# Performance work log

Hardware: AMD Instinct MI355X
Metric: run time of the kernel (lower is better)

Reference implementation:

```python
import jax, jax.numpy as jnp
import numpy as np

B_, T_, IDIM, D, H, FF, L, MAXLEN = 8, 512, 1799, 256, 4, 2048, 16, 1000
DK = D // H


def _ln(x, g, b, eps=1e-12):
    m = jnp.mean(x, axis=-1, keepdims=True)
    v = jnp.mean((x - m) ** 2, axis=-1, keepdims=True)
    return (x - m) * jax.lax.rsqrt(v + eps) * g + b


def setup_inputs() -> dict:
    key = jax.random.key(0)
    ks = jax.random.split(key, 16)
    s = 0.02
    n = lambda k, shape: jax.random.normal(k, shape, jnp.float32) * s
    return {
        'xs': jax.random.normal(ks[0], (B_, T_, IDIM), jnp.float32),
        'masks': jnp.ones((B_, 1, T_), jnp.int32),
        'emb_w': n(ks[1], (D, IDIM)), 'emb_b': jnp.zeros((D,), jnp.float32),
        'emb_g': jnp.ones((D,), jnp.float32), 'emb_beta': jnp.zeros((D,), jnp.float32),
        'pe_k': n(ks[2], (2 * MAXLEN, DK)),
        'Wq': n(ks[3], (L, D, D)), 'bq': jnp.zeros((L, D), jnp.float32),
        'Wk': n(ks[4], (L, D, D)), 'bk': jnp.zeros((L, D), jnp.float32),
        'Wv': n(ks[5], (L, D, D)), 'bv': jnp.zeros((L, D), jnp.float32),
        'Wo': n(ks[6], (L, D, D)), 'bo': jnp.zeros((L, D), jnp.float32),
        'ln1_g': jnp.ones((L, D), jnp.float32), 'ln1_b': jnp.zeros((L, D), jnp.float32),
        'ln2_g': jnp.ones((L, D), jnp.float32), 'ln2_b': jnp.zeros((L, D), jnp.float32),
        'lnk_g': jnp.ones((L, DK), jnp.float32), 'lnk_b': jnp.zeros((L, DK), jnp.float32),
        'W1': n(ks[7], (L, FF, D)), 'b1': jnp.zeros((L, FF), jnp.float32),
        'W2': n(ks[8], (L, D, FF)), 'b2': jnp.zeros((L, D), jnp.float32),
        'after_g': jnp.ones((D,), jnp.float32), 'after_b': jnp.zeros((D,), jnp.float32),
    }


def reference(xs, masks, emb_w, emb_b, emb_g, emb_beta, pe_k, Wq, bq, Wk, bk, Wv, bv, Wo, bo,
              ln1_g, ln1_b, ln2_g, ln2_b, lnk_g, lnk_b, W1, b1, W2, b2, after_g, after_b):
    # embed: Linear -> LayerNorm -> (Dropout=id) -> ReLU
    x = jax.nn.relu(_ln(xs @ emb_w.T + emb_b, emb_g, emb_beta))  # [B,T,D]
    # relative position table gather: pos_k [T,T,DK]
    pos = jnp.arange(T_)
    rel = jnp.clip(pos[:, None] - pos[None, :], -MAXLEN, MAXLEN - 1) + MAXLEN
    pos_k = pe_k[rel]
    neg = (masks == 0)[:, None, :, :]  # [B,1,1,T]
    minval = jnp.finfo(x.dtype).min
    scale = 1.0 / np.sqrt(DK).astype(np.float32)

    def block(x, p):
        y = _ln(x, p['ln1_g'], p['ln1_b'])
        pk = _ln(pos_k, p['lnk_g'], p['lnk_b'])  # norm_k applied per layer
        proj = lambda W, b: (y @ W.T + b).reshape(B_, T_, H, DK).transpose(0, 2, 1, 3)
        q = proj(p['Wq'], p['bq'])  # [B,H,T,DK]
        k = proj(p['Wk'], p['bk'])
        v = proj(p['Wv'], p['bv'])
        A = jnp.einsum('bhtd,bhsd->bhts', q, k)
        Bt = jnp.einsum('bhtd,tsd->bhts', q, pk)  # rel-pos bias term
        scores = jnp.where(neg, minval, (A + Bt) * scale)
        attn = jnp.where(neg, 0.0, jax.nn.softmax(scores, axis=-1))
        o = jnp.einsum('bhts,bhsd->bhtd', attn, v)
        o = o.transpose(0, 2, 1, 3).reshape(B_, T_, D)
        x = x + o @ p['Wo'].T + p['bo']
        y2 = _ln(x, p['ln2_g'], p['ln2_b'])
        ff = jax.nn.relu(y2 @ p['W1'].T + p['b1']) @ p['W2'].T + p['b2']
        return x + ff, None

    params = {'Wq': Wq, 'bq': bq, 'Wk': Wk, 'bk': bk, 'Wv': Wv, 'bv': bv, 'Wo': Wo, 'bo': bo,
              'ln1_g': ln1_g, 'ln1_b': ln1_b, 'ln2_g': ln2_g, 'ln2_b': ln2_b,
              'lnk_g': lnk_g, 'lnk_b': lnk_b, 'W1': W1, 'b1': b1, 'W2': W2, 'b2': b2}
    x, _ = jax.lax.scan(block, x, params)
    return _ln(x, after_g, after_b)
```

## Files before the change

kernel.cpp:

```cpp
#include <hip/hip_runtime.h>
#include <cstdint>


typedef __bf16 bf16_t;
typedef bf16_t bf16x4 __attribute__((ext_vector_type(4)));
typedef bf16_t bf16x8 __attribute__((ext_vector_type(8)));
typedef float  f32x4  __attribute__((ext_vector_type(4)));

#define B_    8
#define T_    512
#define IDIM  1799
#define KPAD  1856
#define D_    256
#define H_    4
#define DK    64
#define FF_   2048
#define L_    16
#define NROW  4096
#define PKROWS 2000
#define NBH   32
#define NSA   4

__device__ __forceinline__ f32x4 mfma16(bf16x8 a, bf16x8 b, f32x4 c) {
  return __builtin_amdgcn_mfma_f32_16x16x32_bf16(a, b, c, 0, 0, 0);
}

__device__ __forceinline__ void async_cp16(const void* g, void* l) {
  __builtin_amdgcn_global_load_lds(
      (__attribute__((address_space(1))) void*)(g),
      (__attribute__((address_space(3))) void*)(l), 16, 0, 0);
}

__global__ __launch_bounds__(256) void cvt_f32_bf16(const float* __restrict__ s,
                                                    bf16_t* __restrict__ d, int n) {
  int i = blockIdx.x * 256 + threadIdx.x;
  int stride = gridDim.x * 256;
  for (; i < n; i += stride) d[i] = (bf16_t)s[i];
}

__global__ __launch_bounds__(256) void cvt_pad_row(const float* __restrict__ s,
                                                   bf16_t* __restrict__ d,
                                                   int ksrc, int kdst) {
  const int r = blockIdx.x;
  const float* sr = s + (size_t)r * ksrc;
  bf16_t* dr = d + (size_t)r * kdst;
  for (int k = threadIdx.x; k < kdst; k += 256)
    dr[k] = (k < ksrc) ? (bf16_t)sr[k] : (bf16_t)0.f;
}

__global__ __launch_bounds__(256) void pack_qkvw(const float* __restrict__ wq,
                                                 const float* __restrict__ wk,
                                                 const float* __restrict__ wv,
                                                 bf16_t* __restrict__ dst) {
  const int per_l = 768 * 256;
  int i = blockIdx.x * 256 + threadIdx.x;
  int stride = gridDim.x * 256;
  for (; i < L_ * per_l; i += stride) {
    int l = i / per_l, r = i - l * per_l;
    int n = r >> 8, c = r & 255;
    int sel = n >> 8, nn = n & 255;
    const float* w = (sel == 0) ? wq : (sel == 1) ? wk : wv;
    dst[i] = (bf16_t)w[((size_t)l * 256 + nn) * 256 + c];
  }
}

__global__ __launch_bounds__(256) void pack_qkvb(const float* __restrict__ bq,
                                                 const float* __restrict__ bk,
                                                 const float* __restrict__ bv,
                                                 float* __restrict__ dst) {
  int i = blockIdx.x * 256 + threadIdx.x;
  if (i >= L_ * 768) return;
  int l = i / 768, n = i - l * 768;
  int sel = n >> 8, nn = n & 255;
  const float* b = (sel == 0) ? bq : (sel == 1) ? bk : bv;
  dst[i] = b[l * 256 + nn];
}

__global__ __launch_bounds__(256) void pkn_ln(const float* __restrict__ pe_k,
                                              const float* __restrict__ lnk_g,
                                              const float* __restrict__ lnk_b,
                                              bf16_t* __restrict__ out) {
  const int idx = blockIdx.x * 4 + (threadIdx.x >> 6);
  if (idx >= L_ * PKROWS) return;
  const int lane = threadIdx.x & 63;
  const int l = idx / PKROWS, r = idx - l * PKROWS;
  float v = pe_k[(size_t)r * DK + lane];
  float s = v;
#pragma unroll
  for (int o = 32; o; o >>= 1) s += __shfl_xor(s, o);
  const float mean = s * (1.f / DK);
  const float dx = v - mean;
  float q = dx * dx;
#pragma unroll
  for (int o = 32; o; o >>= 1) q += __shfl_xor(q, o);
  const float rs = rsqrtf(q * (1.f / DK) + 1e-12f);
  out[((size_t)l * PKROWS + r) * DK + lane] =
      (bf16_t)(dx * rs * lnk_g[l * DK + lane] + lnk_b[l * DK + lane]);
}

template <bool BF16OUT, bool RELU>
__global__ __launch_bounds__(256) void ln_rows(const float* __restrict__ src,
                                               const float* __restrict__ g,
                                               const float* __restrict__ b,
                                               void* __restrict__ dst) {
  const int row = blockIdx.x * 4 + (threadIdx.x >> 6);
  const int lane = threadIdx.x & 63;
  const float4 v = ((const float4*)(src + (size_t)row * D_))[lane];
  float s = v.x + v.y + v.z + v.w;
#pragma unroll
  for (int o = 32; o; o >>= 1) s += __shfl_xor(s, o);
  const float mean = s * (1.f / D_);
  const float d0 = v.x - mean, d1 = v.y - mean, d2 = v.z - mean, d3 = v.w - mean;
  float q = d0 * d0 + d1 * d1 + d2 * d2 + d3 * d3;
#pragma unroll
  for (int o = 32; o; o >>= 1) q += __shfl_xor(q, o);
  const float rs = rsqrtf(q * (1.f / D_) + 1e-12f);
  const float4 gg = ((const float4*)g)[lane];
  const float4 bb = ((const float4*)b)[lane];
  float o0 = d0 * rs * gg.x + bb.x;
  float o1 = d1 * rs * gg.y + bb.y;
  float o2 = d2 * rs * gg.z + bb.z;
  float o3 = d3 * rs * gg.w + bb.w;
  if (RELU) {
    o0 = fmaxf(o0, 0.f); o1 = fmaxf(o1, 0.f);
    o2 = fmaxf(o2, 0.f); o3 = fmaxf(o3, 0.f);
  }
  if (BF16OUT) {
    bf16x4 o4 = {(bf16_t)o0, (bf16_t)o1, (bf16_t)o2, (bf16_t)o3};
    ((bf16x4*)((bf16_t*)dst + (size_t)row * D_))[lane] = o4;
  } else {
    ((float4*)((float*)dst + (size_t)row * D_))[lane] = make_float4(o0, o1, o2, o3);
  }
}

template <int NS, bool WRITE_Y>
__global__ __launch_bounds__(256) void add_combine_ln(
    const float* __restrict__ parts, const float* __restrict__ bias,
    float* __restrict__ x, const float* __restrict__ g,
    const float* __restrict__ b, bf16_t* __restrict__ y) {
  const int row = blockIdx.x * 4 + (threadIdx.x >> 6);
  const int lane = threadIdx.x & 63;
  const size_t idx = (size_t)row * 64 + lane;
  float4 v = ((const float4*)x)[idx];
#pragma unroll
  for (int p = 0; p < NS; ++p) {
    float4 pv = ((const float4*)parts)[(size_t)p * NROW * 64 + idx];
    v.x += pv.x; v.y += pv.y; v.z += pv.z; v.w += pv.w;
  }
  const float4 bi = ((const float4*)bias)[lane];
  v.x += bi.x; v.y += bi.y; v.z += bi.z; v.w += bi.w;
  ((float4*)x)[idx] = v;
  if (WRITE_Y) {
    float s = v.x + v.y + v.z + v.w;
#pragma unroll
    for (int o = 32; o; o >>= 1) s += __shfl_xor(s, o);
    const float mean = s * (1.f / D_);
    const float d0 = v.x - mean, d1 = v.y - mean, d2 = v.z - mean, d3 = v.w - mean;
    float q = d0 * d0 + d1 * d1 + d2 * d2 + d3 * d3;
#pragma unroll
    for (int o = 32; o; o >>= 1) q += __shfl_xor(q, o);
    const float rs = rsqrtf(q * (1.f / D_) + 1e-12f);
    const float4 gg = ((const float4*)g)[lane];
    const float4 bb = ((const float4*)b)[lane];
    bf16x4 o4 = {(bf16_t)(d0 * rs * gg.x + bb.x), (bf16_t)(d1 * rs * gg.y + bb.y),
                 (bf16_t)(d2 * rs * gg.z + bb.z), (bf16_t)(d3 * rs * gg.w + bb.w)};
    ((bf16x4*)y)[idx] = o4;
  }
}

__global__ __launch_bounds__(256) void embed_combine(
    const float* __restrict__ parts, const float* __restrict__ bias,
    const float* __restrict__ g, const float* __restrict__ b,
    float* __restrict__ x) {
  const int row = blockIdx.x * 4 + (threadIdx.x >> 6);
  const int lane = threadIdx.x & 63;
  const size_t idx = (size_t)row * 64 + lane;
  float4 v = ((const float4*)parts)[idx];
  float4 p1 = ((const float4*)parts)[(size_t)NROW * 64 + idx];
  const float4 bi = ((const float4*)bias)[lane];
  v.x += p1.x + bi.x; v.y += p1.y + bi.y; v.z += p1.z + bi.z; v.w += p1.w + bi.w;
  float s = v.x + v.y + v.z + v.w;
#pragma unroll
  for (int o = 32; o; o >>= 1) s += __shfl_xor(s, o);
  const float mean = s * (1.f / D_);
  const float d0 = v.x - mean, d1 = v.y - mean, d2 = v.z - mean, d3 = v.w - mean;
  float q = d0 * d0 + d1 * d1 + d2 * d2 + d3 * d3;
#pragma unroll
  for (int o = 32; o; o >>= 1) q += __shfl_xor(q, o);
  const float rs = rsqrtf(q * (1.f / D_) + 1e-12f);
  const float4 gg = ((const float4*)g)[lane];
  const float4 bb = ((const float4*)b)[lane];
  ((float4*)x)[idx] = make_float4(
      fmaxf(d0 * rs * gg.x + bb.x, 0.f), fmaxf(d1 * rs * gg.y + bb.y, 0.f),
      fmaxf(d2 * rs * gg.z + bb.z, 0.f), fmaxf(d3 * rs * gg.w + bb.w, 0.f));
}

template <int BM, int BN, int EP, int MINW>
__global__ __launch_bounds__(256, MINW) void gemm_bf16(
    const bf16_t* __restrict__ A, int lda, const bf16_t* __restrict__ B, int ldb,
    const float* __restrict__ bias, void* __restrict__ Cout, int ldc,
    const float* __restrict__ resid, int K, size_t zstride) {
  constexpr int HM = BM / 2, HN = BN / 2;
  constexpr int FM = HM / 16, FN = HN / 16;
  constexpr int CA = (BM * 8) / 256, CB = (BN * 8) / 256;
  __shared__ bf16_t lsA[BM * 64];
  __shared__ bf16_t lsB[BN * 64];
  const int tid = threadIdx.x;
  const int w = tid >> 6, lane = tid & 63;
  const int wm = w >> 1, wn = w & 1;
  const int lanelo = lane & 15, quad = lane >> 4;
  const int wbase = tid & ~63;
  const int m0 = blockIdx.x * BM, n0 = blockIdx.y * BN;
  const int ktiles = K >> 6;
  const int tpz = (ktiles + gridDim.z - 1) / gridDim.z;
  const int kb = blockIdx.z * tpz * 64;
  const int ke = min(K, kb + tpz * 64);
  f32x4 acc[FM][FN] = {};

  for (int kt = kb; kt < ke; kt += 64) {
    __syncthreads();
#pragma unroll
    for (int rr = 0; rr < CA; ++rr) {
      int chunk = rr * 256 + tid;
      int r = chunk >> 3, c8 = chunk & 7;
      int lg = c8 ^ (r & 7);
      async_cp16(A + (size_t)(m0 + r) * lda + kt + lg * 8,
                 lsA + (size_t)(rr * 256 + wbase) * 8);
    }
#pragma unroll
    for (int rr = 0; rr < CB; ++rr) {
      int chunk = rr * 256 + tid;
      int r = chunk >> 3, c8 = chunk & 7;
      int lg = c8 ^ (r & 7);
      async_cp16(B + (size_t)(n0 + r) * ldb + kt + lg * 8,
                 lsB + (size_t)(rr * 256 + wbase) * 8);
    }
    __syncthreads();
    bf16x8 af[FM][2], bfv[FN][2];
#pragma unroll
    for (int i = 0; i < FM; ++i) {
      int r = wm * HM + i * 16 + lanelo;
#pragma unroll
      for (int kk = 0; kk < 2; ++kk)
        af[i][kk] = *(const bf16x8*)(lsA + (size_t)(r * 8 + ((kk * 4 + quad) ^ (r & 7))) * 8);
    }
#pragma unroll
    for (int j = 0; j < FN; ++j) {
      int r = wn * HN + j * 16 + lanelo;
#pragma unroll
      for (int kk = 0; kk < 2; ++kk)
        bfv[j][kk] = *(const bf16x8*)(lsB + (size_t)(r * 8 + ((kk * 4 + quad) ^ (r & 7))) * 8);
    }
#pragma unroll
    for (int kk = 0; kk < 2; ++kk)
#pragma unroll
      for (int i = 0; i < FM; ++i)
#pragma unroll
        for (int j = 0; j < FN; ++j)
          acc[i][j] = mfma16(af[i][kk], bfv[j][kk], acc[i][j]);
  }

#pragma unroll
  for (int i = 0; i < FM; ++i) {
#pragma unroll
    for (int j = 0; j < FN; ++j) {
#pragma unroll
      for (int reg = 0; reg < 4; ++reg) {
        const int m = m0 + wm * HM + i * 16 + quad * 4 + reg;
        const int n = n0 + wn * HN + j * 16 + lanelo;
        const size_t idx = (size_t)m * ldc + n;
        if constexpr (EP == 4) {
          ((float*)Cout + (size_t)blockIdx.z * zstride)[idx] = acc[i][j][reg];
        } else {
          float v = acc[i][j][reg] + bias[n];
          if constexpr (EP == 0) {
            ((float*)Cout)[idx] = v;
          } else if constexpr (EP == 1) {
            ((bf16_t*)Cout)[idx] = (bf16_t)v;
          } else if constexpr (EP == 2) {
            ((bf16_t*)Cout)[idx] = (bf16_t)fmaxf(v, 0.f);
          } else {
            ((float*)Cout)[idx] = v + resid[idx];
          }
        }
      }
    }
  }
}

__global__ __launch_bounds__(256, 3) void bt_gemm(
    const bf16_t* __restrict__ qkv, const bf16_t* __restrict__ pkn,
    bf16_t* __restrict__ Bt) {
  __shared__ bf16_t ls_q[64 * 64];
  __shared__ bf16_t ls_j[192 * 64];
  const int tid = threadIdx.x, w = tid >> 6, lane = tid & 63;
  const int wm = w >> 1, wn = w & 1;
  const int lanelo = lane & 15, quad = lane >> 4;
  const int wbase = tid & ~63;
  const int t0 = blockIdx.x * 64;
  const int bh = blockIdx.y, bb = bh >> 2, h = bh & 3;
  const size_t rowbase = (size_t)bb * T_;
  const int relbase = t0 + 489;

#pragma unroll
  for (int rr = 0; rr < 2; ++rr) {
    int chunk = rr * 256 + tid;
    int r = chunk >> 3, c8 = chunk & 7;
    int lg = c8 ^ (r & 7);
    async_cp16(qkv + (rowbase + t0 + r) * 768 + h * 64 + lg * 8,
               ls_q + (size_t)(rr * 256 + wbase) * 8);
  }
  __syncthreads();
  bf16x8 qf[2][2];
#pragma unroll
  for (int i = 0; i < 2; ++i) {
    int r = wm * 32 + i * 16 + lanelo;
#pragma unroll
    for (int kk = 0; kk < 2; ++kk)
      qf[i][kk] = *(const bf16x8*)(ls_q + (size_t)(r * 8 + ((kk * 4 + quad) ^ (r & 7))) * 8);
  }

  for (int jc = 0; jc < 3; ++jc) {
    if (jc) __syncthreads();
#pragma unroll
    for (int rr = 0; rr < 6; ++rr) {
      int chunk = rr * 256 + tid;
      int r = chunk >> 3, c8 = chunk & 7;
      int lg = c8 ^ (r & 7);
      async_cp16(pkn + (size_t)(relbase + jc * 192 + r) * DK + lg * 8,
                 ls_j + (size_t)(rr * 256 + wbase) * 8);
    }
    __syncthreads();
    f32x4 racc[2][6] = {};
#pragma unroll
    for (int kk = 0; kk < 2; ++kk)
#pragma unroll
      for (int nf = 0; nf < 6; ++nf) {
        int r = wn * 96 + nf * 16 + lanelo;
        bf16x8 bj = *(const bf16x8*)(ls_j + (size_t)(r * 8 + ((kk * 4 + quad) ^ (r & 7))) * 8);
#pragma unroll
        for (int i = 0; i < 2; ++i) racc[i][nf] = mfma16(qf[i][kk], bj, racc[i][nf]);
      }
#pragma unroll
    for (int i = 0; i < 2; ++i)
#pragma unroll
      for (int nf = 0; nf < 6; ++nf)
#pragma unroll
        for (int reg = 0; reg < 4; ++reg) {
          const int tl = wm * 32 + i * 16 + quad * 4 + reg;
          const int jj = jc * 192 + wn * 96 + nf * 16 + lanelo;
          const int s = tl + 511 - jj;
          if (s >= 0 && s < T_)
            Bt[(((size_t)bh * T_ + t0 + tl) << 9) + s] = (bf16_t)racc[i][nf][reg];
        }
  }
}

__global__ __launch_bounds__(256, 4) void attn_part(
    const bf16_t* __restrict__ qkv, const bf16_t* __restrict__ Bt,
    const int* __restrict__ masks, bf16_t* __restrict__ Opart,
    float* __restrict__ mpart, float* __restrict__ lpart) {
  __shared__ bf16_t ls_q[64 * 64];
  __shared__ bf16_t ls_k[64 * 64];
  __shared__ bf16_t ls_vt[64 * 72];
  __shared__ bf16_t ls_p[64 * 72];

  const int tid = threadIdx.x, w = tid >> 6, lane = tid & 63;
  const int lanelo = lane & 15, quad = lane >> 4;
  const int wbase = tid & ~63;
  const int t0 = blockIdx.x * 64;
  const int bh = blockIdx.y, bb = bh >> 2, h = bh & 3;
  const int z = blockIdx.z;
  const size_t rowbase = (size_t)bb * T_;

#pragma unroll
  for (int rr = 0; rr < 2; ++rr) {
    int chunk = rr * 256 + tid;
    int r = chunk >> 3, c8 = chunk & 7;
    int lg = c8 ^ (r & 7);
    async_cp16(qkv + (rowbase + t0 + r) * 768 + h * 64 + lg * 8,
               ls_q + (size_t)(rr * 256 + wbase) * 8);
  }
  __syncthreads();
  bf16x8 qf[2];
#pragma unroll
  for (int kk = 0; kk < 2; ++kk) {
    int r = w * 16 + lanelo;
    qf[kk] = *(const bf16x8*)(ls_q + (size_t)(r * 8 + ((kk * 4 + quad) ^ (r & 7))) * 8);
  }

  f32x4 o_acc[4] = {};
  float m_run[4], l_run[4];
#pragma unroll
  for (int i = 0; i < 4; ++i) { m_run[i] = -__builtin_inff(); l_run[i] = 0.f; }

  for (int st = 2 * z; st < 2 * z + 2; ++st) {
    const int s0 = st * 64;
    __syncthreads();
#pragma unroll
    for (int rr = 0; rr < 2; ++rr) {
      int chunk = rr * 256 + tid;
      int r = chunk >> 3, c8 = chunk & 7;
      int lg = c8 ^ (r & 7);
      async_cp16(qkv + (rowbase + s0 + r) * 768 + 256 + h * 64 + lg * 8,
                 ls_k + (size_t)(rr * 256 + wbase) * 8);
    }
#pragma unroll
    for (int c = tid; c < 64 * 8; c += 256) {
      int r = c & 63, d0 = (c >> 6) * 8;
      bf16x8 vv = *(const bf16x8*)(qkv + (rowbase + s0 + r) * 768 + 512 + h * 64 + d0);
#pragma unroll
      for (int i = 0; i < 8; ++i) ls_vt[(d0 + i) * 72 + r] = vv[i];
    }
    __syncthreads();

    float btv[4][4];
    int mk[4];
#pragma unroll
    for (int nf = 0; nf < 4; ++nf) {
      const int scol = nf * 16 + lanelo;
      mk[nf] = masks[bb * T_ + s0 + scol];
#pragma unroll
      for (int reg = 0; reg < 4; ++reg) {
        const int trow = w * 16 + quad * 4 + reg;
        btv[nf][reg] = (float)Bt[(((size_t)bh * T_ + t0 + trow) << 9) + s0 + scol];
      }
    }
    f32x4 sacc[4] = {};
#pragma unroll
    for (int kk = 0; kk < 2; ++kk)
#pragma unroll
      for (int nf = 0; nf < 4; ++nf) {
        int r = nf * 16 + lanelo;
        bf16x8 bk = *(const bf16x8*)(ls_k + (size_t)(r * 8 + ((kk * 4 + quad) ^ (r & 7))) * 8);
        sacc[nf] = mfma16(qf[kk], bk, sacc[nf]);
      }
    float sv[4][4];
#pragma unroll
    for (int nf = 0; nf < 4; ++nf)
#pragma unroll
      for (int reg = 0; reg < 4; ++reg)
        sv[nf][reg] = mk[nf] ? (sacc[nf][reg] + btv[nf][reg]) * 0.125f
                             : -3.4028235e38f;
    float alpha[4];
#pragma unroll
    for (int reg = 0; reg < 4; ++reg) {
      float bm = fmaxf(fmaxf(sv[0][reg], sv[1][reg]), fmaxf(sv[2][reg], sv[3][reg]));
#pragma unroll
      for (int o = 1; o < 16; o <<= 1) bm = fmaxf(bm, __shfl_xor(bm, o));
      const float mn = fmaxf(m_run[reg], bm);
      alpha[reg] = __expf(m_run[reg] - mn);
      m_run[reg] = mn;
      float rsum = 0.f;
#pragma unroll
      for (int nf = 0; nf < 4; ++nf) {
        float p = __expf(sv[nf][reg] - mn) * (mk[nf] ? 1.f : 0.f);
        sv[nf][reg] = p;
        rsum += p;
      }
#pragma unroll
      for (int o = 1; o < 16; o <<= 1) rsum += __shfl_xor(rsum, o);
      l_run[reg] = l_run[reg] * alpha[reg] + rsum;
    }
#pragma unroll
    for (int nf = 0; nf < 4; ++nf)
#pragma unroll
      for (int reg = 0; reg < 4; ++reg) {
        o_acc[nf][reg] *= alpha[reg];
        ls_p[(w * 16 + quad * 4 + reg) * 72 + nf * 16 + lanelo] = (bf16_t)sv[nf][reg];
      }
#pragma unroll
    for (int kk = 0; kk < 2; ++kk) {
      bf16x8 ap = *(const bf16x8*)&ls_p[(w * 16 + lanelo) * 72 + kk * 32 + quad * 8];
#pragma unroll
      for (int nf = 0; nf < 4; ++nf) {
        bf16x8 bv = *(const bf16x8*)&ls_vt[(nf * 16 + lanelo) * 72 + kk * 32 + quad * 8];
        o_acc[nf] = mfma16(ap, bv, o_acc[nf]);
      }
    }
  }

#pragma unroll
  for (int reg = 0; reg < 4; ++reg) {
    const int trow = w * 16 + quad * 4 + reg;
    const size_t prow = ((size_t)z * NBH + bh) * T_ + t0 + trow;
#pragma unroll
    for (int nf = 0; nf < 4; ++nf)
      Opart[prow * 64 + nf * 16 + lanelo] = (bf16_t)o_acc[nf][reg];
    if (lanelo == 0) { mpart[prow] = m_run[reg]; lpart[prow] = l_run[reg]; }
  }
}

__global__ __launch_bounds__(256) void attn_combine(
    const bf16_t* __restrict__ Opart, const float* __restrict__ mpart,
    const float* __restrict__ lpart, bf16_t* __restrict__ ao) {
  const int hr = blockIdx.x * 4 + (threadIdx.x >> 6);
  const int lane = threadIdx.x & 63;
  const int bh = hr >> 9, t = hr & 511;
  float mp[NSA], lp[NSA];
  float m = -__builtin_inff();
#pragma unroll
  for (int p = 0; p < NSA; ++p) {
    const size_t prow = ((size_t)p * NBH + bh) * T_ + t;
    mp[p] = mpart[prow]; lp[p] = lpart[prow];
    m = fmaxf(m, mp[p]);
  }
  float denom = 0.f, o = 0.f;
#pragma unroll
  for (int p = 0; p < NSA; ++p) {
    if (lp[p] > 0.f) {
      const float wp = __expf(mp[p] - m);
      denom += lp[p] * wp;
      o += (float)Opart[(((size_t)p * NBH + bh) * T_ + t) * 64 + lane] * wp;
    }
  }
  const float res = (denom > 0.f) ? o / denom : 0.f;
  const int bb = bh >> 2, hh = bh & 3;
  ao[((size_t)bb * T_ + t) * D_ + hh * 64 + lane] = (bf16_t)res;
}

extern "C" void kernel_launch(void* const* d_in, const int* in_sizes, int n_in,
                              void* d_out, int out_size, void* d_ws, size_t ws_size,
                              hipStream_t stream) {
  const float* xs       = (const float*)d_in[0];
  const int*   masks    = (const int*)d_in[1];
  const float* emb_w    = (const float*)d_in[2];
  const float* emb_b    = (const float*)d_in[3];
  const float* emb_g    = (const float*)d_in[4];
  const float* emb_beta = (const float*)d_in[5];
  const float* pe_k     = (const float*)d_in[6];
  const float* Wq       = (const float*)d_in[7];
  const float* bq       = (const float*)d_in[8];
  const float* Wk       = (const float*)d_in[9];
  const float* bk       = (const float*)d_in[10];
  const float* Wv       = (const float*)d_in[11];
  const float* bv       = (const float*)d_in[12];
  const float* Wo       = (const float*)d_in[13];
  const float* bo       = (const float*)d_in[14];
  const float* ln1_g    = (const float*)d_in[15];
  const float* ln1_b    = (const float*)d_in[16];
  const float* ln2_g    = (const float*)d_in[17];
  const float* ln2_b    = (const float*)d_in[18];
  const float* lnk_g    = (const float*)d_in[19];
  const float* lnk_b    = (const float*)d_in[20];
  const float* W1       = (const float*)d_in[21];
  const float* b1       = (const float*)d_in[22];
  const float* W2       = (const float*)d_in[23];
  const float* b2       = (const float*)d_in[24];
  const float* after_g  = (const float*)d_in[25];
  const float* after_b  = (const float*)d_in[26];

  char* ws = (char*)d_ws;
  size_t off = 0;
  auto take = [&](size_t bytes) -> void* {
    void* p = ws + off;
    off += (bytes + 255) & ~(size_t)255;
    return p;
  };
  bf16_t* ewb  = (bf16_t*)take((size_t)D_ * KPAD * 2);
  bf16_t* wcat = (bf16_t*)take((size_t)L_ * 768 * D_ * 2);
  float*  bcat = (float*) take((size_t)L_ * 768 * 4);
  bf16_t* wob  = (bf16_t*)take((size_t)L_ * D_ * D_ * 2);
  bf16_t* w1b  = (bf16_t*)take((size_t)L_ * FF_ * D_ * 2);
  bf16_t* w2b  = (bf16_t*)take((size_t)L_ * D_ * FF_ * 2);
  bf16_t* pknb = (bf16_t*)take((size_t)L_ * PKROWS * DK * 2);
  float*  x    = (float*) take((size_t)NROW * D_ * 4);
  bf16_t* y    = (bf16_t*)take((size_t)NROW * D_ * 2);
  bf16_t* qkv  = (bf16_t*)take((size_t)NROW * 768 * 2);
  bf16_t* ao   = (bf16_t*)take((size_t)NROW * D_ * 2);
  bf16_t* hbuf = (bf16_t*)take((size_t)NROW * FF_ * 2);
  bf16_t* Btb  = (bf16_t*)take((size_t)NBH * T_ * T_ * 2);
  bf16_t* Opart = (bf16_t*)take((size_t)NSA * NBH * T_ * 64 * 2);
  float*  mpart = (float*)take((size_t)NSA * NBH * T_ * 4);
  float*  lpart = (float*)take((size_t)NSA * NBH * T_ * 4);
  float*  gpart = (float*)take((size_t)2 * NROW * D_ * 4);
  bf16_t* xsb  = hbuf;
  const size_t ZS = (size_t)NROW * D_;

  cvt_pad_row<<<NROW, 256, 0, stream>>>(xs, xsb, IDIM, KPAD);
  cvt_pad_row<<<D_, 256, 0, stream>>>(emb_w, ewb, IDIM, KPAD);
  pack_qkvw<<<2048, 256, 0, stream>>>(Wq, Wk, Wv, wcat);
  pack_qkvb<<<48, 256, 0, stream>>>(bq, bk, bv, bcat);
  cvt_f32_bf16<<<1024, 256, 0, stream>>>(Wo, wob, L_ * D_ * D_);
  cvt_f32_bf16<<<2048, 256, 0, stream>>>(W1, w1b, L_ * FF_ * D_);
  cvt_f32_bf16<<<2048, 256, 0, stream>>>(W2, w2b, L_ * D_ * FF_);
  pkn_ln<<<(L_ * PKROWS) / 4, 256, 0, stream>>>(pe_k, lnk_g, lnk_b, pknb);

  gemm_bf16<64, 64, 4, 3><<<dim3(NROW / 64, D_ / 64, 2), 256, 0, stream>>>(
      xsb, KPAD, ewb, KPAD, nullptr, gpart, D_, nullptr, KPAD, ZS);
  embed_combine<<<NROW / 4, 256, 0, stream>>>(gpart, emb_b, emb_g, emb_beta, x);
  ln_rows<true, false><<<NROW / 4, 256, 0, stream>>>(x, ln1_g, ln1_b, y);

  for (int l = 0; l < L_; ++l) {
    gemm_bf16<64, 64, 1, 3><<<dim3(NROW / 64, 768 / 64), 256, 0, stream>>>(
        y, D_, wcat + (size_t)l * 768 * D_, D_, bcat + l * 768, qkv, 768, nullptr,
        D_, 0);
    bt_gemm<<<dim3(T_ / 64, NBH), 256, 0, stream>>>(
        qkv, pknb + (size_t)l * PKROWS * DK, Btb);
    attn_part<<<dim3(T_ / 64, NBH, NSA), 256, 0, stream>>>(
        qkv, Btb, masks, Opart, mpart, lpart);
    attn_combine<<<NBH * T_ / 4, 256, 0, stream>>>(Opart, mpart, lpart, ao);
    gemm_bf16<64, 64, 4, 3><<<dim3(NROW / 64, D_ / 64, 2), 256, 0, stream>>>(
        ao, D_, wob + (size_t)l * D_ * D_, D_, nullptr, gpart, D_, nullptr, D_, ZS);
    add_combine_ln<2, true><<<NROW / 4, 256, 0, stream>>>(
        gpart, bo + l * D_, x, ln2_g + l * D_, ln2_b + l * D_, y);
    gemm_bf16<128, 128, 2, 2><<<dim3(NROW / 128, FF_ / 128), 256, 0, stream>>>(
        y, D_, w1b + (size_t)l * FF_ * D_, D_, b1 + l * FF_, hbuf, FF_, nullptr,
        D_, 0);
    gemm_bf16<64, 64, 4, 3><<<dim3(NROW / 64, D_ / 64, 2), 256, 0, stream>>>(
        hbuf, FF_, w2b + (size_t)l * D_ * FF_, FF_, nullptr, gpart, D_, nullptr,
        FF_, ZS);
    if (l < L_ - 1) {
      add_combine_ln<2, true><<<NROW / 4, 256, 0, stream>>>(
          gpart, b2 + l * D_, x, ln1_g + (l + 1) * D_, ln1_b + (l + 1) * D_, y);
    } else {
      add_combine_ln<2, false><<<NROW / 4, 256, 0, stream>>>(
          gpart, b2 + l * D_, x, nullptr, nullptr, nullptr);
    }
  }
  ln_rows<false, false><<<NROW / 4, 256, 0, stream>>>(x, after_g, after_b,
                                                      (float*)d_out);
}
```

Baseline: 1.436 ms.

## Fuse rel-pos bias into attention, fold combine into Wo GEMM, retile GEMMs

```diff
diff --git a/kernel.cpp b/kernel.cpp
--- a/kernel.cpp
+++ b/kernel.cpp
@@ -98,11 +98,10 @@
       (bf16_t)(dx * rs * lnk_g[l * DK + lane] + lnk_b[l * DK + lane]);
 }
 
-template <bool BF16OUT, bool RELU>
-__global__ __launch_bounds__(256) void ln_rows(const float* __restrict__ src,
-                                               const float* __restrict__ g,
-                                               const float* __restrict__ b,
-                                               void* __restrict__ dst) {
+__global__ __launch_bounds__(256) void ln_rows_f32(const float* __restrict__ src,
+                                                   const float* __restrict__ g,
+                                                   const float* __restrict__ b,
+                                                   float* __restrict__ dst) {
   const int row = blockIdx.x * 4 + (threadIdx.x >> 6);
   const int lane = threadIdx.x & 63;
   const float4 v = ((const float4*)(src + (size_t)row * D_))[lane];
@@ -117,20 +116,9 @@
   const float rs = rsqrtf(q * (1.f / D_) + 1e-12f);
   const float4 gg = ((const float4*)g)[lane];
   const float4 bb = ((const float4*)b)[lane];
-  float o0 = d0 * rs * gg.x + bb.x;
-  float o1 = d1 * rs * gg.y + bb.y;
-  float o2 = d2 * rs * gg.z + bb.z;
-  float o3 = d3 * rs * gg.w + bb.w;
-  if (RELU) {
-    o0 = fmaxf(o0, 0.f); o1 = fmaxf(o1, 0.f);
-    o2 = fmaxf(o2, 0.f); o3 = fmaxf(o3, 0.f);
-  }
-  if (BF16OUT) {
-    bf16x4 o4 = {(bf16_t)o0, (bf16_t)o1, (bf16_t)o2, (bf16_t)o3};
-    ((bf16x4*)((bf16_t*)dst + (size_t)row * D_))[lane] = o4;
-  } else {
-    ((float4*)((float*)dst + (size_t)row * D_))[lane] = make_float4(o0, o1, o2, o3);
-  }
+  ((float4*)(dst + (size_t)row * D_))[lane] =
+      make_float4(d0 * rs * gg.x + bb.x, d1 * rs * gg.y + bb.y,
+                  d2 * rs * gg.z + bb.z, d3 * rs * gg.w + bb.w);
 }
 
 template <int NS, bool WRITE_Y>
@@ -170,36 +158,57 @@
 
 __global__ __launch_bounds__(256) void embed_combine(
     const float* __restrict__ parts, const float* __restrict__ bias,
-    const float* __restrict__ g, const float* __restrict__ b,
-    float* __restrict__ x) {
+    const float* __restrict__ g0, const float* __restrict__ b0,
+    const float* __restrict__ g1, const float* __restrict__ b1,
+    float* __restrict__ x, bf16_t* __restrict__ y) {
   const int row = blockIdx.x * 4 + (threadIdx.x >> 6);
   const int lane = threadIdx.x & 63;
   const size_t idx = (size_t)row * 64 + lane;
   float4 v = ((const float4*)parts)[idx];
-  float4 p1 = ((const float4*)parts)[(size_t)NROW * 64 + idx];
+#pragma unroll
+  for (int p = 1; p < 4; ++p) {
+    float4 pv = ((const float4*)parts)[(size_t)p * NROW * 64 + idx];
+    v.x += pv.x; v.y += pv.y; v.z += pv.z; v.w += pv.w;
+  }
   const float4 bi = ((const float4*)bias)[lane];
-  v.x += p1.x + bi.x; v.y += p1.y + bi.y; v.z += p1.z + bi.z; v.w += p1.w + bi.w;
+  v.x += bi.x; v.y += bi.y; v.z += bi.z; v.w += bi.w;
   float s = v.x + v.y + v.z + v.w;
 #pragma unroll
   for (int o = 32; o; o >>= 1) s += __shfl_xor(s, o);
-  const float mean = s * (1.f / D_);
-  const float d0 = v.x - mean, d1 = v.y - mean, d2 = v.z - mean, d3 = v.w - mean;
+  float mean = s * (1.f / D_);
+  float d0 = v.x - mean, d1 = v.y - mean, d2 = v.z - mean, d3 = v.w - mean;
   float q = d0 * d0 + d1 * d1 + d2 * d2 + d3 * d3;
 #pragma unroll
   for (int o = 32; o; o >>= 1) q += __shfl_xor(q, o);
-  const float rs = rsqrtf(q * (1.f / D_) + 1e-12f);
-  const float4 gg = ((const float4*)g)[lane];
-  const float4 bb = ((const float4*)b)[lane];
-  ((float4*)x)[idx] = make_float4(
-      fmaxf(d0 * rs * gg.x + bb.x, 0.f), fmaxf(d1 * rs * gg.y + bb.y, 0.f),
-      fmaxf(d2 * rs * gg.z + bb.z, 0.f), fmaxf(d3 * rs * gg.w + bb.w, 0.f));
+  float rs = rsqrtf(q * (1.f / D_) + 1e-12f);
+  const float4 gg = ((const float4*)g0)[lane];
+  const float4 bb = ((const float4*)b0)[lane];
+  float x0 = fmaxf(d0 * rs * gg.x + bb.x, 0.f);
+  float x1 = fmaxf(d1 * rs * gg.y + bb.y, 0.f);
+  float x2 = fmaxf(d2 * rs * gg.z + bb.z, 0.f);
+  float x3 = fmaxf(d3 * rs * gg.w + bb.w, 0.f);
+  ((float4*)x)[idx] = make_float4(x0, x1, x2, x3);
+  s = x0 + x1 + x2 + x3;
+#pragma unroll
+  for (int o = 32; o; o >>= 1) s += __shfl_xor(s, o);
+  mean = s * (1.f / D_);
+  d0 = x0 - mean; d1 = x1 - mean; d2 = x2 - mean; d3 = x3 - mean;
+  q = d0 * d0 + d1 * d1 + d2 * d2 + d3 * d3;
+#pragma unroll
+  for (int o = 32; o; o >>= 1) q += __shfl_xor(q, o);
+  rs = rsqrtf(q * (1.f / D_) + 1e-12f);
+  const float4 g1v = ((const float4*)g1)[lane];
+  const float4 b1v = ((const float4*)b1)[lane];
+  bf16x4 o4 = {(bf16_t)(d0 * rs * g1v.x + b1v.x), (bf16_t)(d1 * rs * g1v.y + b1v.y),
+               (bf16_t)(d2 * rs * g1v.z + b1v.z), (bf16_t)(d3 * rs * g1v.w + b1v.w)};
+  ((bf16x4*)y)[idx] = o4;
 }
 
 template <int BM, int BN, int EP, int MINW>
 __global__ __launch_bounds__(256, MINW) void gemm_bf16(
     const bf16_t* __restrict__ A, int lda, const bf16_t* __restrict__ B, int ldb,
     const float* __restrict__ bias, void* __restrict__ Cout, int ldc,
-    const float* __restrict__ resid, int K, size_t zstride) {
+    int K, size_t zstride) {
   constexpr int HM = BM / 2, HN = BN / 2;
   constexpr int FM = HM / 16, FN = HN / 16;
   constexpr int CA = (BM * 8) / 256, CB = (BN * 8) / 256;
@@ -273,14 +282,10 @@
           ((float*)Cout + (size_t)blockIdx.z * zstride)[idx] = acc[i][j][reg];
         } else {
           float v = acc[i][j][reg] + bias[n];
-          if constexpr (EP == 0) {
-            ((float*)Cout)[idx] = v;
-          } else if constexpr (EP == 1) {
+          if constexpr (EP == 1) {
             ((bf16_t*)Cout)[idx] = (bf16_t)v;
-          } else if constexpr (EP == 2) {
+          } else {
             ((bf16_t*)Cout)[idx] = (bf16_t)fmaxf(v, 0.f);
-          } else {
-            ((float*)Cout)[idx] = v + resid[idx];
           }
         }
       }
@@ -288,82 +293,114 @@
   }
 }
 
-__global__ __launch_bounds__(256, 3) void bt_gemm(
-    const bf16_t* __restrict__ qkv, const bf16_t* __restrict__ pkn,
-    bf16_t* __restrict__ Bt) {
-  __shared__ bf16_t ls_q[64 * 64];
-  __shared__ bf16_t ls_j[192 * 64];
-  const int tid = threadIdx.x, w = tid >> 6, lane = tid & 63;
+__global__ __launch_bounds__(256, 2) void wo_gemm(
+    const bf16_t* __restrict__ Opart, const float* __restrict__ mpart,
+    const float* __restrict__ lpart, const bf16_t* __restrict__ B,
+    float* __restrict__ Cout, size_t zstride) {
+  __shared__ bf16_t lsA[64 * 64];
+  __shared__ bf16_t lsB[128 * 64];
+  const int tid = threadIdx.x;
+  const int w = tid >> 6, lane = tid & 63;
   const int wm = w >> 1, wn = w & 1;
   const int lanelo = lane & 15, quad = lane >> 4;
   const int wbase = tid & ~63;
-  const int t0 = blockIdx.x * 64;
-  const int bh = blockIdx.y, bb = bh >> 2, h = bh & 3;
-  const size_t rowbase = (size_t)bb * T_;
-  const int relbase = t0 + 489;
-
-#pragma unroll
-  for (int rr = 0; rr < 2; ++rr) {
-    int chunk = rr * 256 + tid;
-    int r = chunk >> 3, c8 = chunk & 7;
-    int lg = c8 ^ (r & 7);
-    async_cp16(qkv + (rowbase + t0 + r) * 768 + h * 64 + lg * 8,
-               ls_q + (size_t)(rr * 256 + wbase) * 8);
-  }
-  __syncthreads();
-  bf16x8 qf[2][2];
-#pragma unroll
-  for (int i = 0; i < 2; ++i) {
-    int r = wm * 32 + i * 16 + lanelo;
-#pragma unroll
-    for (int kk = 0; kk < 2; ++kk)
-      qf[i][kk] = *(const bf16x8*)(ls_q + (size_t)(r * 8 + ((kk * 4 + quad) ^ (r & 7))) * 8);
-  }
-
-  for (int jc = 0; jc < 3; ++jc) {
-    if (jc) __syncthreads();
-#pragma unroll
-    for (int rr = 0; rr < 6; ++rr) {
+  const int m0 = blockIdx.x * 64, n0 = blockIdx.y * 128;
+  const int z = blockIdx.z;
+  const int bb = m0 >> 9, t0 = m0 & 511;
+  f32x4 acc[2][4] = {};
+
+  for (int kt = z * 128; kt < z * 128 + 128; kt += 64) {
+    __syncthreads();
+    const int hh = kt >> 6;
+    const int bh = bb * 4 + hh;
+#pragma unroll
+    for (int rr = 0; rr < 2; ++rr) {
+      int chunk = rr * 256 + tid;
+      int r = chunk >> 3, c8 = chunk & 7;
+      int dk0 = (c8 ^ (r & 7)) * 8;
+      int t = t0 + r;
+      float mp[NSA], lp[NSA];
+      float mmax = -__builtin_inff();
+#pragma unroll
+      for (int p = 0; p < NSA; ++p) {
+        const size_t prow = ((size_t)p * NBH + bh) * T_ + t;
+        mp[p] = mpart[prow]; lp[p] = lpart[prow];
+        mmax = fmaxf(mmax, mp[p]);
+      }
+      float e[NSA], denom = 0.f;
+#pragma unroll
+      for (int p = 0; p < NSA; ++p) {
+        e[p] = __expf(mp[p] - mmax);
+        denom += lp[p] * e[p];
+      }
+      const float inv = (denom > 0.f) ? 1.f / denom : 0.f;
+      float cv[8] = {};
+#pragma unroll
+      for (int p = 0; p < NSA; ++p) {
+        const float wgt = e[p] * inv;
+        bf16x8 op = *(const bf16x8*)(Opart +
+            (((size_t)p * NBH + bh) * T_ + t) * 64 + dk0);
+#pragma unroll
+        for (int i = 0; i < 8; ++i) cv[i] += wgt * (float)op[i];
+      }
+      bf16x8 rv;
+#pragma unroll
+      for (int i = 0; i < 8; ++i) rv[i] = (bf16_t)cv[i];
+      *(bf16x8*)(lsA + (size_t)chunk * 8) = rv;
+    }
+#pragma unroll
+    for (int rr = 0; rr < 4; ++rr) {
       int chunk = rr * 256 + tid;
       int r = chunk >> 3, c8 = chunk & 7;
       int lg = c8 ^ (r & 7);
-      async_cp16(pkn + (size_t)(relbase + jc * 192 + r) * DK + lg * 8,
-                 ls_j + (size_t)(rr * 256 + wbase) * 8);
+      async_cp16(B + (size_t)(n0 + r) * 256 + kt + lg * 8,
+                 lsB + (size_t)(rr * 256 + wbase) * 8);
     }
     __syncthreads();
-    f32x4 racc[2][6] = {};
+    bf16x8 af[2][2], bfv[4][2];
+#pragma unroll
+    for (int i = 0; i < 2; ++i) {
+      int r = wm * 32 + i * 16 + lanelo;
+#pragma unroll
+      for (int kk = 0; kk < 2; ++kk)
+        af[i][kk] = *(const bf16x8*)(lsA + (size_t)(r * 8 + ((kk * 4 + quad) ^ (r & 7))) * 8);
+    }
+#pragma unroll
+    for (int j = 0; j < 4; ++j) {
+      int r = wn * 64 + j * 16 + lanelo;
+#pragma unroll
+      for (int kk = 0; kk < 2; ++kk)
+        bfv[j][kk] = *(const bf16x8*)(lsB + (size_t)(r * 8 + ((kk * 4 + quad) ^ (r & 7))) * 8);
+    }
 #pragma unroll
     for (int kk = 0; kk < 2; ++kk)
 #pragma unroll
-      for (int nf = 0; nf < 6; ++nf) {
-        int r = wn * 96 + nf * 16 + lanelo;
-        bf16x8 bj = *(const bf16x8*)(ls_j + (size_t)(r * 8 + ((kk * 4 + quad) ^ (r & 7))) * 8);
-#pragma unroll
-        for (int i = 0; i < 2; ++i) racc[i][nf] = mfma16(qf[i][kk], bj, racc[i][nf]);
-      }
-#pragma unroll
-    for (int i = 0; i < 2; ++i)
-#pragma unroll
-      for (int nf = 0; nf < 6; ++nf)
-#pragma unroll
-        for (int reg = 0; reg < 4; ++reg) {
-          const int tl = wm * 32 + i * 16 + quad * 4 + reg;
-          const int jj = jc * 192 + wn * 96 + nf * 16 + lanelo;
-          const int s = tl + 511 - jj;
-          if (s >= 0 && s < T_)
-            Bt[(((size_t)bh * T_ + t0 + tl) << 9) + s] = (bf16_t)racc[i][nf][reg];
-        }
-  }
-}
-
-__global__ __launch_bounds__(256, 4) void attn_part(
-    const bf16_t* __restrict__ qkv, const bf16_t* __restrict__ Bt,
+      for (int i = 0; i < 2; ++i)
+#pragma unroll
+        for (int j = 0; j < 4; ++j)
+          acc[i][j] = mfma16(af[i][kk], bfv[j][kk], acc[i][j]);
+  }
+
+#pragma unroll
+  for (int i = 0; i < 2; ++i)
+#pragma unroll
+    for (int j = 0; j < 4; ++j)
+#pragma unroll
+      for (int reg = 0; reg < 4; ++reg) {
+        const int m = m0 + wm * 32 + i * 16 + quad * 4 + reg;
+        const int n = n0 + wn * 64 + j * 16 + lanelo;
+        (Cout + (size_t)z * zstride)[(size_t)m * D_ + n] = acc[i][j][reg];
+      }
+}
+
+__global__ __launch_bounds__(256, 3) void attn_fused(
+    const bf16_t* __restrict__ qkv, const bf16_t* __restrict__ pkn,
     const int* __restrict__ masks, bf16_t* __restrict__ Opart,
     float* __restrict__ mpart, float* __restrict__ lpart) {
-  __shared__ bf16_t ls_q[64 * 64];
+  __shared__ bf16_t ls_qp[64 * 72];
+  __shared__ bf16_t ls_pkr[64 * 196];
   __shared__ bf16_t ls_k[64 * 64];
   __shared__ bf16_t ls_vt[64 * 72];
-  __shared__ bf16_t ls_p[64 * 72];
 
   const int tid = threadIdx.x, w = tid >> 6, lane = tid & 63;
   const int lanelo = lane & 15, quad = lane >> 4;
@@ -372,6 +409,7 @@
   const int bh = blockIdx.y, bb = bh >> 2, h = bh & 3;
   const int z = blockIdx.z;
   const size_t rowbase = (size_t)bb * T_;
+  const int jb = t0 - 128 * z + 873;
 
 #pragma unroll
   for (int rr = 0; rr < 2; ++rr) {
@@ -379,23 +417,47 @@
     int r = chunk >> 3, c8 = chunk & 7;
     int lg = c8 ^ (r & 7);
     async_cp16(qkv + (rowbase + t0 + r) * 768 + h * 64 + lg * 8,
-               ls_q + (size_t)(rr * 256 + wbase) * 8);
+               ls_qp + (size_t)(rr * 256 + wbase) * 8);
+  }
+#pragma unroll
+  for (int rr = 0; rr < 6; ++rr) {
+    int chunk = rr * 256 + tid;
+    int r = chunk >> 3, c8 = chunk & 7;
+    int lg = c8 ^ (r & 7);
+    async_cp16(pkn + (size_t)(jb + r) * DK + lg * 8,
+               ls_pkr + (size_t)(rr * 256 + wbase) * 8);
   }
   __syncthreads();
   bf16x8 qf[2];
 #pragma unroll
   for (int kk = 0; kk < 2; ++kk) {
     int r = w * 16 + lanelo;
-    qf[kk] = *(const bf16x8*)(ls_q + (size_t)(r * 8 + ((kk * 4 + quad) ^ (r & 7))) * 8);
-  }
+    qf[kk] = *(const bf16x8*)(ls_qp + (size_t)(r * 8 + ((kk * 4 + quad) ^ (r & 7))) * 8);
+  }
+  f32x4 racc[12] = {};
+#pragma unroll
+  for (int kk = 0; kk < 2; ++kk)
+#pragma unroll
+    for (int nf = 0; nf < 12; ++nf) {
+      int r = nf * 16 + lanelo;
+      bf16x8 bj = *(const bf16x8*)(ls_pkr + (size_t)(r * 8 + ((kk * 4 + quad) ^ (r & 7))) * 8);
+      racc[nf] = mfma16(qf[kk], bj, racc[nf]);
+    }
+  __syncthreads();
+#pragma unroll
+  for (int nf = 0; nf < 12; ++nf)
+#pragma unroll
+    for (int reg = 0; reg < 4; ++reg)
+      ls_pkr[(w * 16 + quad * 4 + reg) * 196 + nf * 16 + lanelo] =
+          (bf16_t)racc[nf][reg];
 
   f32x4 o_acc[4] = {};
   float m_run[4], l_run[4];
 #pragma unroll
   for (int i = 0; i < 4; ++i) { m_run[i] = -__builtin_inff(); l_run[i] = 0.f; }
 
-  for (int st = 2 * z; st < 2 * z + 2; ++st) {
-    const int s0 = st * 64;
+  for (int stl = 0; stl < 2; ++stl) {
+    const int s0 = 128 * z + 64 * stl;
     __syncthreads();
 #pragma unroll
     for (int rr = 0; rr < 2; ++rr) {
@@ -412,20 +474,12 @@
 #pragma unroll
       for (int i = 0; i < 8; ++i) ls_vt[(d0 + i) * 72 + r] = vv[i];
     }
+    int mk[4];
+#pragma unroll
+    for (int nf = 0; nf < 4; ++nf)
+      mk[nf] = masks[bb * T_ + s0 + nf * 16 + lanelo];
     __syncthreads();
 
-    float btv[4][4];
-    int mk[4];
-#pragma unroll
-    for (int nf = 0; nf < 4; ++nf) {
-      const int scol = nf * 16 + lanelo;
-      mk[nf] = masks[bb * T_ + s0 + scol];
-#pragma unroll
-      for (int reg = 0; reg < 4; ++reg) {
-        const int trow = w * 16 + quad * 4 + reg;
-        btv[nf][reg] = (float)Bt[(((size_t)bh * T_ + t0 + trow) << 9) + s0 + scol];
-      }
-    }
     f32x4 sacc[4] = {};
 #pragma unroll
     for (int kk = 0; kk < 2; ++kk)
@@ -437,11 +491,15 @@
       }
     float sv[4][4];
 #pragma unroll
-    for (int nf = 0; nf < 4; ++nf)
-#pragma unroll
-      for (int reg = 0; reg < 4; ++reg)
-        sv[nf][reg] = mk[nf] ? (sacc[nf][reg] + btv[nf][reg]) * 0.125f
-                             : -3.4028235e38f;
+    for (int nf = 0; nf < 4; ++nf) {
+      const int scol = nf * 16 + lanelo;
+#pragma unroll
+      for (int reg = 0; reg < 4; ++reg) {
+        const int trow = w * 16 + quad * 4 + reg;
+        const float bt = (float)ls_pkr[trow * 196 + (trow - scol - 64 * stl + 127)];
+        sv[nf][reg] = mk[nf] ? (sacc[nf][reg] + bt) * 0.125f : -3.4028235e38f;
+      }
+    }
     float alpha[4];
 #pragma unroll
     for (int reg = 0; reg < 4; ++reg) {
@@ -467,11 +525,11 @@
 #pragma unroll
       for (int reg = 0; reg < 4; ++reg) {
         o_acc[nf][reg] *= alpha[reg];
-        ls_p[(w * 16 + quad * 4 + reg) * 72 + nf * 16 + lanelo] = (bf16_t)sv[nf][reg];
+        ls_qp[(w * 16 + quad * 4 + reg) * 72 + nf * 16 + lanelo] = (bf16_t)sv[nf][reg];
       }
 #pragma unroll
     for (int kk = 0; kk < 2; ++kk) {
-      bf16x8 ap = *(const bf16x8*)&ls_p[(w * 16 + lanelo) * 72 + kk * 32 + quad * 8];
+      bf16x8 ap = *(const bf16x8*)&ls_qp[(w * 16 + lanelo) * 72 + kk * 32 + quad * 8];
 #pragma unroll
       for (int nf = 0; nf < 4; ++nf) {
         bf16x8 bv = *(const bf16x8*)&ls_vt[(nf * 16 + lanelo) * 72 + kk * 32 + quad * 8];
@@ -489,34 +547,6 @@
       Opart[prow * 64 + nf * 16 + lanelo] = (bf16_t)o_acc[nf][reg];
     if (lanelo == 0) { mpart[prow] = m_run[reg]; lpart[prow] = l_run[reg]; }
   }
-}
-
-__global__ __launch_bounds__(256) void attn_combine(
-    const bf16_t* __restrict__ Opart, const float* __restrict__ mpart,
-    const float* __restrict__ lpart, bf16_t* __restrict__ ao) {
-  const int hr = blockIdx.x * 4 + (threadIdx.x >> 6);
-  const int lane = threadIdx.x & 63;
-  const int bh = hr >> 9, t = hr & 511;
-  float mp[NSA], lp[NSA];
-  float m = -__builtin_inff();
-#pragma unroll
-  for (int p = 0; p < NSA; ++p) {
-    const size_t prow = ((size_t)p * NBH + bh) * T_ + t;
-    mp[p] = mpart[prow]; lp[p] = lpart[prow];
-    m = fmaxf(m, mp[p]);
-  }
-  float denom = 0.f, o = 0.f;
-#pragma unroll
-  for (int p = 0; p < NSA; ++p) {
-    if (lp[p] > 0.f) {
-      const float wp = __expf(mp[p] - m);
-      denom += lp[p] * wp;
-      o += (float)Opart[(((size_t)p * NBH + bh) * T_ + t) * 64 + lane] * wp;
-    }
-  }
-  const float res = (denom > 0.f) ? o / denom : 0.f;
-  const int bb = bh >> 2, hh = bh & 3;
-  ao[((size_t)bb * T_ + t) * D_ + hh * 64 + lane] = (bf16_t)res;
 }
 
 extern "C" void kernel_launch(void* const* d_in, const int* in_sizes, int n_in,
@@ -567,13 +597,11 @@
   float*  x    = (float*) take((size_t)NROW * D_ * 4);
   bf16_t* y    = (bf16_t*)take((size_t)NROW * D_ * 2);
   bf16_t* qkv  = (bf16_t*)take((size_t)NROW * 768 * 2);
-  bf16_t* ao   = (bf16_t*)take((size_t)NROW * D_ * 2);
   bf16_t* hbuf = (bf16_t*)take((size_t)NROW * FF_ * 2);
-  bf16_t* Btb  = (bf16_t*)take((size_t)NBH * T_ * T_ * 2);
   bf16_t* Opart = (bf16_t*)take((size_t)NSA * NBH * T_ * 64 * 2);
   float*  mpart = (float*)take((size_t)NSA * NBH * T_ * 4);
   float*  lpart = (float*)take((size_t)NSA * NBH * T_ * 4);
-  float*  gpart = (float*)take((size_t)2 * NROW * D_ * 4);
+  float*  gpart = (float*)take((size_t)4 * NROW * D_ * 4);
   bf16_t* xsb  = hbuf;
   const size_t ZS = (size_t)NROW * D_;
 
@@ -586,38 +614,31 @@
   cvt_f32_bf16<<<2048, 256, 0, stream>>>(W2, w2b, L_ * D_ * FF_);
   pkn_ln<<<(L_ * PKROWS) / 4, 256, 0, stream>>>(pe_k, lnk_g, lnk_b, pknb);
 
-  gemm_bf16<64, 64, 4, 3><<<dim3(NROW / 64, D_ / 64, 2), 256, 0, stream>>>(
-      xsb, KPAD, ewb, KPAD, nullptr, gpart, D_, nullptr, KPAD, ZS);
-  embed_combine<<<NROW / 4, 256, 0, stream>>>(gpart, emb_b, emb_g, emb_beta, x);
-  ln_rows<true, false><<<NROW / 4, 256, 0, stream>>>(x, ln1_g, ln1_b, y);
+  gemm_bf16<128, 128, 4, 2><<<dim3(NROW / 128, D_ / 128, 4), 256, 0, stream>>>(
+      xsb, KPAD, ewb, KPAD, nullptr, gpart, D_, KPAD, ZS);
+  embed_combine<<<NROW / 4, 256, 0, stream>>>(gpart, emb_b, emb_g, emb_beta,
+                                              ln1_g, ln1_b, x, y);
 
   for (int l = 0; l < L_; ++l) {
-    gemm_bf16<64, 64, 1, 3><<<dim3(NROW / 64, 768 / 64), 256, 0, stream>>>(
-        y, D_, wcat + (size_t)l * 768 * D_, D_, bcat + l * 768, qkv, 768, nullptr,
-        D_, 0);
-    bt_gemm<<<dim3(T_ / 64, NBH), 256, 0, stream>>>(
-        qkv, pknb + (size_t)l * PKROWS * DK, Btb);
-    attn_part<<<dim3(T_ / 64, NBH, NSA), 256, 0, stream>>>(
-        qkv, Btb, masks, Opart, mpart, lpart);
-    attn_combine<<<NBH * T_ / 4, 256, 0, stream>>>(Opart, mpart, lpart, ao);
-    gemm_bf16<64, 64, 4, 3><<<dim3(NROW / 64, D_ / 64, 2), 256, 0, stream>>>(
-        ao, D_, wob + (size_t)l * D_ * D_, D_, nullptr, gpart, D_, nullptr, D_, ZS);
+    gemm_bf16<64, 128, 1, 3><<<dim3(NROW / 64, 768 / 128), 256, 0, stream>>>(
+        y, D_, wcat + (size_t)l * 768 * D_, D_, bcat + l * 768, qkv, 768, D_, 0);
+    attn_fused<<<dim3(T_ / 64, NBH, NSA), 256, 0, stream>>>(
+        qkv, pknb + (size_t)l * PKROWS * DK, masks, Opart, mpart, lpart);
+    wo_gemm<<<dim3(NROW / 64, D_ / 128, 2), 256, 0, stream>>>(
+        Opart, mpart, lpart, wob + (size_t)l * D_ * D_, gpart, ZS);
     add_combine_ln<2, true><<<NROW / 4, 256, 0, stream>>>(
         gpart, bo + l * D_, x, ln2_g + l * D_, ln2_b + l * D_, y);
     gemm_bf16<128, 128, 2, 2><<<dim3(NROW / 128, FF_ / 128), 256, 0, stream>>>(
-        y, D_, w1b + (size_t)l * FF_ * D_, D_, b1 + l * FF_, hbuf, FF_, nullptr,
-        D_, 0);
-    gemm_bf16<64, 64, 4, 3><<<dim3(NROW / 64, D_ / 64, 2), 256, 0, stream>>>(
-        hbuf, FF_, w2b + (size_t)l * D_ * FF_, FF_, nullptr, gpart, D_, nullptr,
-        FF_, ZS);
+        y, D_, w1b + (size_t)l * FF_ * D_, D_, b1 + l * FF_, hbuf, FF_, D_, 0);
+    gemm_bf16<128, 128, 4, 2><<<dim3(NROW / 128, D_ / 128, 4), 256, 0, stream>>>(
+        hbuf, FF_, w2b + (size_t)l * D_ * FF_, FF_, nullptr, gpart, D_, FF_, ZS);
     if (l < L_ - 1) {
-      add_combine_ln<2, true><<<NROW / 4, 256, 0, stream>>>(
+      add_combine_ln<4, true><<<NROW / 4, 256, 0, stream>>>(
           gpart, b2 + l * D_, x, ln1_g + (l + 1) * D_, ln1_b + (l + 1) * D_, y);
     } else {
-      add_combine_ln<2, false><<<NROW / 4, 256, 0, stream>>>(
+      add_combine_ln<4, false><<<NROW / 4, 256, 0, stream>>>(
           gpart, b2 + l * D_, x, nullptr, nullptr, nullptr);
     }
   }
-  ln_rows<false, false><<<NROW / 4, 256, 0, stream>>>(x, after_g, after_b,
-                                                      (float*)d_out);
-}
+  ln_rows_f32<<<NROW / 4, 256, 0, stream>>>(x, after_g, after_b, (float*)d_out);
+}
```

New measurement: 1.333 ms. 1.08x faster.
